# Kernel optimization log

Hardware: AMD Instinct MI355X
Metric: run time of the kernel (lower is better)

Reference implementation:

```python
import jax, jax.numpy as jnp
import numpy as np

N = 65536   # total nodes
E = 1048576 # total edges (avg degree 16)
B = 512     # graphs in batch
H = 4       # gat1 heads
C = 64      # per-head channels / GNN_HIDDEN


def segment_softmax(logits, seg, num_segments):
    # numerically stable softmax over segments (PyG softmax semantics, eps=1e-16)
    m = jax.ops.segment_max(logits, seg, num_segments=num_segments)
    m = jnp.where(jnp.isfinite(m), m, 0.0)
    e = jnp.exp(logits - m[seg])
    s = jax.ops.segment_sum(e, seg, num_segments=num_segments)
    return e / (s[seg] + 1e-16)


def gat_conv(x, edge_index, edge_attr, W, att_src, att_dst, We, att_edge, bias, heads, out_ch, concat):
    # PyG GATConv with edge_dim, add_self_loops=False
    n = x.shape[0]
    h = (x @ W).reshape(n, heads, out_ch)                 # (N,H,C)
    src, dst = edge_index[0], edge_index[1]
    a_s = jnp.sum(h * att_src, axis=-1)                   # (N,H)
    a_d = jnp.sum(h * att_dst, axis=-1)                   # (N,H)
    he = (edge_attr @ We).reshape(-1, heads, out_ch)      # (E,H,C)
    a_e = jnp.sum(he * att_edge, axis=-1)                 # (E,H)
    alpha = jax.nn.leaky_relu(a_s[src] + a_d[dst] + a_e, negative_slope=0.2)
    alpha = segment_softmax(alpha, dst, n)                # softmax over incoming edges per dst
    out = jax.ops.segment_sum(h[src] * alpha[..., None], dst, num_segments=n)  # (N,H,C)
    out = out.reshape(n, heads * out_ch) if concat else out.mean(axis=1)
    return out + bias


def setup_inputs() -> dict:
    key = jax.random.key(0)
    ks = jax.random.split(key, 24)
    s = 0.05
    d = {}
    d["global_feat"] = jax.random.normal(ks[0], (B, 512), jnp.float32)
    d["x"] = jax.random.normal(ks[1], (N, 13), jnp.float32)
    d["roi_feats"] = jax.random.normal(ks[2], (N, 256), jnp.float32)
    d["edge_index"] = jax.random.randint(ks[3], (2, E), 0, N)
    d["edge_attr"] = jax.random.normal(ks[4], (E, 5), jnp.float32)
    d["batch_vec"] = jnp.sort(jax.random.randint(ks[5], (N,), 0, B))
    # roi_proj / scene_proj
    d["roi_W"] = jax.random.normal(ks[6], (256, 64), jnp.float32) * s
    d["roi_b"] = jnp.zeros((64,), jnp.float32)
    d["scene_W"] = jax.random.normal(ks[7], (512, 128), jnp.float32) * s
    d["scene_b"] = jnp.zeros((128,), jnp.float32)
    d["g1_W"] = jax.random.normal(ks[8], (77, H * C), jnp.float32) * s
    d["g1_att_src"] = jax.random.normal(ks[9], (H, C), jnp.float32) * s
    d["g1_att_dst"] = jax.random.normal(ks[10], (H, C), jnp.float32) * s
    d["g1_We"] = jax.random.normal(ks[11], (5, H * C), jnp.float32) * s
    d["g1_att_edge"] = jax.random.normal(ks[12], (H, C), jnp.float32) * s
    d["g1_bias"] = jnp.zeros((H * C,), jnp.float32)
    # gat2: 256 -> 64, 1 head
    d["g2_W"] = jax.random.normal(ks[13], (H * C, C), jnp.float32) * s
    d["g2_att_src"] = jax.random.normal(ks[14], (1, C), jnp.float32) * s
    d["g2_att_dst"] = jax.random.normal(ks[15], (1, C), jnp.float32) * s
    d["g2_We"] = jax.random.normal(ks[16], (5, C), jnp.float32) * s
    d["g2_att_edge"] = jax.random.normal(ks[17], (1, C), jnp.float32) * s
    d["g2_bias"] = jnp.zeros((C,), jnp.float32)
    # attention pooling gate + classifier
    d["gate_W"] = jax.random.normal(ks[18], (C, 1), jnp.float32) * s
    d["gate_b"] = jnp.zeros((1,), jnp.float32)
    d["cls1_W"] = jax.random.normal(ks[19], (128 + C, 64), jnp.float32) * s
    d["cls1_b"] = jnp.zeros((64,), jnp.float32)
    d["cls2_W"] = jax.random.normal(ks[20], (64, 3), jnp.float32) * s
    d["cls2_b"] = jnp.zeros((3,), jnp.float32)
    return d


def reference(global_feat, x, roi_feats, edge_index, edge_attr, batch_vec,
              roi_W, roi_b, scene_W, scene_b,
              g1_W, g1_att_src, g1_att_dst, g1_We, g1_att_edge, g1_bias,
              g2_W, g2_att_src, g2_att_dst, g2_We, g2_att_edge, g2_bias,
              gate_W, gate_b, cls1_W, cls1_b, cls2_W, cls2_b):
    scene = global_feat @ scene_W + scene_b                       # (B,128)
    vis = jax.nn.relu(roi_feats @ roi_W + roi_b)                  # (N,64)
    h = jnp.concatenate([x, vis], axis=-1)                        # (N,77)
    h = jax.nn.relu(gat_conv(h, edge_index, edge_attr, g1_W, g1_att_src, g1_att_dst, g1_We, g1_att_edge, g1_bias, H, C, True))
    h = gat_conv(h, edge_index, edge_attr, g2_W, g2_att_src, g2_att_dst, g2_We, g2_att_edge, g2_bias, 1, C, False)  # (N,64)
    # GlobalAttention pooling
    gate = segment_softmax((h @ gate_W + gate_b)[:, 0], batch_vec, B)
    rel = jax.ops.segment_sum(gate[:, None] * h, batch_vec, num_segments=B)  # (B,64)
    comb = jnp.concatenate([scene, rel], axis=-1)                 # (B,192)
    hid = jax.nn.relu(comb @ cls1_W + cls1_b)                     # dropout off (eval)
    return hid @ cls2_W + cls2_b                                  # (B,3)
```

## Files before the change

kernel.cpp:

```cpp
#include <hip/hip_runtime.h>

#define N_NODES 65536
#define N_EDGES 1048576
#define NB      512

typedef unsigned short u16;
typedef unsigned int   u32;
typedef unsigned long long u64;

typedef __attribute__((ext_vector_type(8))) short bf16x8;
typedef __attribute__((ext_vector_type(4))) float f32x4;

__device__ __forceinline__ float bf2f(u16 u) { return __uint_as_float(((u32)u) << 16); }
__device__ __forceinline__ float lo16(u32 u) { return __uint_as_float(u << 16); }
__device__ __forceinline__ float hi16(u32 u) { return __uint_as_float(u & 0xffff0000u); }
__device__ __forceinline__ u16 f2bf(float f) {
    u32 u = __float_as_uint(f);
    u32 r = (u + 0x7fffu + ((u >> 16) & 1u)) >> 16;
    return (u16)r;
}
__device__ __forceinline__ u32 pk2(float a, float b) {
    return (u32)f2bf(a) | ((u32)f2bf(b) << 16);
}
__device__ __forceinline__ float wsum(float v) {
    for (int o = 32; o; o >>= 1) v += __shfl_xor(v, o, 64);
    return v;
}
__device__ __forceinline__ float wmax(float v) {
    for (int o = 32; o; o >>= 1) v = fmaxf(v, __shfl_xor(v, o, 64));
    return v;
}

__global__ void k_prep(const float* g1We, const float* g1ae, const float* g2We, const float* g2ae,
                       float* M1, float* M2) {
    int t = threadIdx.x;
    if (t < 20) {
        int j = t >> 2, h = t & 3;
        float s = 0.f;
        for (int c = 0; c < 64; c++) s += g1We[j * 256 + h * 64 + c] * g1ae[h * 64 + c];
        M1[t] = s;
    } else if (t < 25) {
        int j = t - 20;
        float s = 0.f;
        for (int c = 0; c < 64; c++) s += g2We[j * 64 + c] * g2ae[c];
        M2[j] = s;
    }
}

__global__ void k_wt1(const float* __restrict__ g1W, u16* __restrict__ Wt) {
    int c = blockIdx.x;
    int k = threadIdx.x;
    float v = 0.f;
    if (k < 77) {
        int ko = (k < 64) ? (13 + k) : (k - 64);
        v = g1W[(size_t)ko * 256 + c];
    }
    Wt[(size_t)c * 96 + k] = f2bf(v);
}

__global__ void k_wtv(const float* __restrict__ W, u16* __restrict__ Wt) {
    int c = blockIdx.x;
    int k = threadIdx.x;
    Wt[(size_t)c * 256 + k] = f2bf(W[(size_t)k * 64 + c]);
}

__global__ __launch_bounds__(256) void k_scene(const float* __restrict__ gf, const float* __restrict__ W,
                                               const float* __restrict__ bias, float* __restrict__ scene) {
    int idx = blockIdx.x * 256 + threadIdx.x;
    int b = idx >> 7, j = idx & 127;
    float acc = 0.f;
    for (int k = 0; k < 512; k++) acc += gf[b * 512 + k] * W[k * 128 + j];
    scene[idx] = acc + bias[j];
}

__global__ __launch_bounds__(256) void k_hist(const int* ei, int* cnt) {
    int e = blockIdx.x * 256 + threadIdx.x;
    atomicAdd(&cnt[ei[N_EDGES + e]], 1);
}

__global__ __launch_bounds__(256) void k_scan_blk(const int* __restrict__ cnt, int* __restrict__ pre,
                                                  int* __restrict__ bsum) {
    __shared__ int sd[256];
    int t = threadIdx.x, b = blockIdx.x;
    int base = b * 1024 + t * 4;
    int4 c = *(const int4*)(cnt + base);
    int s = c.x + c.y + c.z + c.w;
    sd[t] = s;
    __syncthreads();
    for (int off = 1; off < 256; off <<= 1) {
        int v = (t >= off) ? sd[t - off] : 0;
        __syncthreads();
        sd[t] += v;
        __syncthreads();
    }
    int excl = sd[t] - s;
    int4 p;
    p.x = excl;
    p.y = excl + c.x;
    p.z = excl + c.x + c.y;
    p.w = excl + c.x + c.y + c.z;
    *(int4*)(pre + base) = p;
    if (t == 255) bsum[b] = sd[255];
}

__global__ __launch_bounds__(64) void k_scan_top(int* bsum) {
    int t = threadIdx.x;
    int v = bsum[t];
    int inc = v;
    for (int off = 1; off < 64; off <<= 1) {
        int u = __shfl_up(inc, off, 64);
        if (t >= off) inc += u;
    }
    bsum[t] = inc - v;
}

__global__ __launch_bounds__(256) void k_scan_fix(const int* __restrict__ pre, const int* __restrict__ bsum,
                                                  int* __restrict__ row_ptr, int* __restrict__ coarse_cur) {
    int i = blockIdx.x * 256 + threadIdx.x;
    int v = pre[i] + bsum[i >> 10];
    row_ptr[i] = v;
    if ((i & 255) == 0) coarse_cur[i >> 8] = v;
    if (i == 0) row_ptr[N_NODES] = N_EDGES;
}

__global__ __launch_bounds__(256) void k_bucket(const int* __restrict__ ei, int* coarse_cur,
                                                u32* __restrict__ bpack, int* __restrict__ bsrc) {
    __shared__ u32 stageP[4096];
    __shared__ int stageS[4096];
    __shared__ int bcnt[256], bscan[256], boff[256], gbase[256];
    int t = threadIdx.x;
    int e0 = blockIdx.x * 4096;
    bcnt[t] = 0;
    __syncthreads();
    int dreg[16], sreg[16];
    for (int it = 0; it < 16; it++) {
        int e = e0 + it * 256 + t;
        int dd = ei[N_EDGES + e];
        dreg[it] = dd;
        sreg[it] = ei[e];
        atomicAdd(&bcnt[dd >> 8], 1);
    }
    __syncthreads();
    int v = bcnt[t];
    bscan[t] = v;
    __syncthreads();
    for (int off = 1; off < 256; off <<= 1) {
        int u = (t >= off) ? bscan[t - off] : 0;
        __syncthreads();
        bscan[t] += u;
        __syncthreads();
    }
    boff[t] = bscan[t] - v;
    gbase[t] = v ? atomicAdd(&coarse_cur[t], v) : 0;
    __syncthreads();
    for (int it = 0; it < 16; it++) {
        int e = e0 + it * 256 + t;
        int b = dreg[it] >> 8;
        int pos = atomicAdd(&boff[b], 1);
        stageP[pos] = ((u32)e << 12) | (u32)(dreg[it] & 255);
        stageS[pos] = sreg[it];
    }
    __syncthreads();
    for (int idx = t; idx < 4096; idx += 256) {
        int lo = 0, hi = 255;
        while (lo < hi) { int mid = (lo + hi) >> 1; if (bscan[mid] > idx) hi = mid; else lo = mid + 1; }
        int b = lo;
        int g = gbase[b] + (idx - (bscan[b] - bcnt[b]));
        bpack[g] = stageP[idx];
        bsrc[g] = stageS[idx];
    }
}

__global__ __launch_bounds__(256) void k_sortb(const u32* __restrict__ bpack, const int* __restrict__ bsrc,
                                               const int* __restrict__ row_ptr,
                                               int* __restrict__ eord, int* __restrict__ ssrc) {
    __shared__ int cur[256];
    int t = threadIdx.x, b = blockIdx.x;
    int nbase = b * 256;
    cur[t] = row_ptr[nbase + t];
    __syncthreads();
    int beg = row_ptr[nbase];
    int end = row_ptr[nbase + 256];
    for (int i = beg + t; i < end; i += 256) {
        u32 wd = bpack[i];
        int src = bsrc[i];
        int d8 = wd & 255;
        int pos = atomicAdd(&cur[d8], 1);
        eord[pos] = (int)(wd >> 12);
        ssrc[pos] = src;
    }
}

__global__ __launch_bounds__(256) void k_payload(const int* __restrict__ eord, const float* __restrict__ ea,
                                                 const float* __restrict__ M1, const float* __restrict__ M2,
                                                 float* __restrict__ a1es, float* __restrict__ a2es) {
    int pos = blockIdx.x * 256 + threadIdx.x;
    int e = eord[pos];
    float v[5];
    for (int j = 0; j < 5; j++) v[j] = ea[(size_t)e * 5 + j];
    float4 o;
    o.x = v[0]*M1[0]  + v[1]*M1[4]  + v[2]*M1[8]  + v[3]*M1[12] + v[4]*M1[16];
    o.y = v[0]*M1[1]  + v[1]*M1[5]  + v[2]*M1[9]  + v[3]*M1[13] + v[4]*M1[17];
    o.z = v[0]*M1[2]  + v[1]*M1[6]  + v[2]*M1[10] + v[3]*M1[14] + v[4]*M1[18];
    o.w = v[0]*M1[3]  + v[1]*M1[7]  + v[2]*M1[11] + v[3]*M1[15] + v[4]*M1[19];
    *(float4*)(a1es + (size_t)pos * 4) = o;
    a2es[pos] = v[0]*M2[0] + v[1]*M2[1] + v[2]*M2[2] + v[3]*M2[3] + v[4]*M2[4];
}

__global__ __launch_bounds__(256) void k_vis(const float* __restrict__ roi, const u16* __restrict__ Wt,
                                             const float* __restrict__ bias, u16* __restrict__ out) {
    __shared__ u16 At[64][264];
    int t = threadIdx.x;
    int w = t >> 6, l = t & 63, lo = l & 15, hi = l >> 4;
    int n0 = blockIdx.x * 64;
    int r = t >> 2, sub = t & 3;
    const float* rp = roi + (size_t)(n0 + r) * 256 + sub * 4;
    #pragma unroll
    for (int q = 0; q < 16; q++) {
        float4 v = *(const float4*)(rp + q * 16);
        uint2 p;
        p.x = pk2(v.x, v.y);
        p.y = pk2(v.z, v.w);
        *(uint2*)&At[r][q * 16 + sub * 4] = p;
    }
    float bb[4][4];
    #pragma unroll
    for (int cb = 0; cb < 4; cb++)
        #pragma unroll
        for (int rg = 0; rg < 4; rg++) bb[cb][rg] = bias[cb * 16 + hi * 4 + rg];
    __syncthreads();
    f32x4 acc[4];
    #pragma unroll
    for (int cb = 0; cb < 4; cb++) acc[cb] = (f32x4){0.f, 0.f, 0.f, 0.f};
    #pragma unroll
    for (int ks = 0; ks < 8; ks++) {
        bf16x8 af = *(const bf16x8*)(&At[w * 16 + lo][ks * 32 + hi * 8]);
        #pragma unroll
        for (int cb = 0; cb < 4; cb++) {
            bf16x8 wf = *(const bf16x8*)(Wt + (size_t)(cb * 16 + lo) * 256 + ks * 32 + hi * 8);
            acc[cb] = __builtin_amdgcn_mfma_f32_16x16x32_bf16(wf, af, acc[cb], 0, 0, 0);
        }
    }
    int nrow = n0 + w * 16 + lo;
    #pragma unroll
    for (int cb = 0; cb < 4; cb++) {
        uint2 p;
        p.x = pk2(fmaxf(acc[cb][0] + bb[cb][0], 0.f), fmaxf(acc[cb][1] + bb[cb][1], 0.f));
        p.y = pk2(fmaxf(acc[cb][2] + bb[cb][2], 0.f), fmaxf(acc[cb][3] + bb[cb][3], 0.f));
        *(uint2*)(out + (size_t)nrow * 64 + cb * 16 + hi * 4) = p;
    }
}

__global__ __launch_bounds__(256) void k_h1(const float* __restrict__ x, const u16* __restrict__ vis,
                                            const u16* __restrict__ Wt,
                                            const float* __restrict__ as_, const float* __restrict__ ad_,
                                            u16* __restrict__ h1, float* __restrict__ a1s,
                                            float* __restrict__ a1d) {
    __shared__ u16 At[64][104];
    int t = threadIdx.x;
    int w = t >> 6, l = t & 63, lo = l & 15, hi = l >> 4;
    int n0 = blockIdx.x * 64;
    int r = t >> 2, sub = t & 3;
    {
        const uint4* vp = (const uint4*)(vis + (size_t)(n0 + r) * 64 + sub * 16);
        uint4 v0 = vp[0], v1 = vp[1];
        *(uint4*)&At[r][sub * 16] = v0;
        *(uint4*)&At[r][sub * 16 + 8] = v1;
        if (sub == 0) {
            const float* xp = x + (size_t)(n0 + r) * 13;
            #pragma unroll
            for (int j = 0; j < 13; j++) At[r][64 + j] = f2bf(xp[j]);
        } else if (sub == 1) {
            #pragma unroll
            for (int j = 77; j < 96; j++) At[r][j] = 0;
        }
    }
    bf16x8 wf[4][3];
    float asv[4][4], adv[4][4];
    #pragma unroll
    for (int cb = 0; cb < 4; cb++) {
        #pragma unroll
        for (int ks = 0; ks < 3; ks++)
            wf[cb][ks] = *(const bf16x8*)(Wt + (size_t)(w * 64 + cb * 16 + lo) * 96 + ks * 32 + hi * 8);
        #pragma unroll
        for (int rg = 0; rg < 4; rg++) {
            asv[cb][rg] = as_[w * 64 + cb * 16 + hi * 4 + rg];
            adv[cb][rg] = ad_[w * 64 + cb * 16 + hi * 4 + rg];
        }
    }
    __syncthreads();
    #pragma unroll
    for (int nb = 0; nb < 4; nb++) {
        f32x4 acc[4];
        #pragma unroll
        for (int cb = 0; cb < 4; cb++) acc[cb] = (f32x4){0.f, 0.f, 0.f, 0.f};
        #pragma unroll
        for (int ks = 0; ks < 3; ks++) {
            bf16x8 af = *(const bf16x8*)(&At[nb * 16 + lo][ks * 32 + hi * 8]);
            #pragma unroll
            for (int cb = 0; cb < 4; cb++)
                acc[cb] = __builtin_amdgcn_mfma_f32_16x16x32_bf16(wf[cb][ks], af, acc[cb], 0, 0, 0);
        }
        int nrow = n0 + nb * 16 + lo;
        float ps = 0.f, pd = 0.f;
        #pragma unroll
        for (int cb = 0; cb < 4; cb++) {
            uint2 p;
            p.x = pk2(acc[cb][0], acc[cb][1]);
            p.y = pk2(acc[cb][2], acc[cb][3]);
            *(uint2*)(h1 + (size_t)nrow * 256 + w * 64 + cb * 16 + hi * 4) = p;
            ps += acc[cb][0] * asv[cb][0] + acc[cb][1] * asv[cb][1]
                + acc[cb][2] * asv[cb][2] + acc[cb][3] * asv[cb][3];
            pd += acc[cb][0] * adv[cb][0] + acc[cb][1] * adv[cb][1]
                + acc[cb][2] * adv[cb][2] + acc[cb][3] * adv[cb][3];
        }
        ps += __shfl_xor(ps, 16, 64); ps += __shfl_xor(ps, 32, 64);
        pd += __shfl_xor(pd, 16, 64); pd += __shfl_xor(pd, 32, 64);
        if (hi == 0) {
            a1s[nrow * 4 + w] = ps;
            a1d[nrow * 4 + w] = pd;
        }
    }
}

__global__ __launch_bounds__(256) void k_h2(const u16* __restrict__ A, const u16* __restrict__ Wt,
                                            const float* __restrict__ as_, const float* __restrict__ ad_,
                                            u16* __restrict__ out, float* __restrict__ a2s,
                                            float* __restrict__ a2d) {
    int t = threadIdx.x;
    int w = t >> 6, l = t & 63, lo = l & 15, hi = l >> 4;
    int nrow = blockIdx.x * 64 + w * 16 + lo;
    f32x4 acc[4];
    #pragma unroll
    for (int cb = 0; cb < 4; cb++) acc[cb] = (f32x4){0.f, 0.f, 0.f, 0.f};
    const u16* ap = A + (size_t)nrow * 256 + hi * 8;
    #pragma unroll
    for (int ks = 0; ks < 8; ks++) {
        bf16x8 af = *(const bf16x8*)(ap + ks * 32);
        #pragma unroll
        for (int cb = 0; cb < 4; cb++) {
            bf16x8 wf = *(const bf16x8*)(Wt + (size_t)(cb * 16 + lo) * 256 + ks * 32 + hi * 8);
            acc[cb] = __builtin_amdgcn_mfma_f32_16x16x32_bf16(wf, af, acc[cb], 0, 0, 0);
        }
    }
    float ps = 0.f, pd = 0.f;
    #pragma unroll
    for (int cb = 0; cb < 4; cb++) {
        uint2 p;
        p.x = pk2(acc[cb][0], acc[cb][1]);
        p.y = pk2(acc[cb][2], acc[cb][3]);
        *(uint2*)(out + (size_t)nrow * 64 + cb * 16 + hi * 4) = p;
        #pragma unroll
        for (int rg = 0; rg < 4; rg++) {
            float a = acc[cb][rg];
            ps += a * as_[cb * 16 + hi * 4 + rg];
            pd += a * ad_[cb * 16 + hi * 4 + rg];
        }
    }
    ps += __shfl_xor(ps, 16, 64); ps += __shfl_xor(ps, 32, 64);
    pd += __shfl_xor(pd, 16, 64); pd += __shfl_xor(pd, 32, 64);
    if (hi == 0) {
        a2s[nrow] = ps;
        a2d[nrow] = pd;
    }
}

__global__ __launch_bounds__(256) void k_sg1(const int* __restrict__ row_ptr, const int* __restrict__ ssrc,
                                             const float* __restrict__ a1s, const float* __restrict__ a1d,
                                             const float* __restrict__ a1es, const u16* __restrict__ h1,
                                             const float* __restrict__ bias, u16* __restrict__ out1) {
    __shared__ float wl[4][1024];
    int t = threadIdx.x;
    int wv = t >> 6, L = t & 63;
    int n = blockIdx.x * 4 + wv;
    int beg = row_ptr[n], deg = row_ptr[n + 1] - beg;
    int lim = (deg < 256) ? deg : 256;
    {
        int h = L >> 4, j = L & 15;
        float adn = a1d[n * 4 + h];
        float m = -3.0e38f, s = 0.f;
        for (int i = j; i < deg; i += 16) {
            int pos = beg + i;
            float l = a1s[ssrc[pos] * 4 + h] + adn + a1es[(size_t)pos * 4 + h];
            l = (l > 0.f) ? l : 0.2f * l;
            if (i < 256) wl[wv][i * 4 + h] = l;
            if (l > m) { s = s * __expf(m - l) + 1.f; m = l; }
            else       { s += __expf(l - m); }
        }
        for (int o = 1; o < 16; o <<= 1) {
            float mo = __shfl_xor(m, o, 64), so = __shfl_xor(s, o, 64);
            float M = fmaxf(m, mo);
            s = s * __expf(m - M) + so * __expf(mo - M);
            m = M;
        }
        float inv = 1.f / (s + 1e-16f);
        for (int i = j; i < lim; i += 16)
            wl[wv][i * 4 + h] = __expf(wl[wv][i * 4 + h] - m) * inv;
    }
    __syncthreads();
    int halfE = L >> 5;
    int L32 = L & 31;
    int hd = L32 >> 3;
    float acc[8];
    #pragma unroll
    for (int j = 0; j < 8; j++) acc[j] = 0.f;
    int last = beg + deg - 1;
    for (int i = 0; i < deg; i += 8) {
        int iA = i + halfE, iB = i + 2 + halfE, iC = i + 4 + halfE, iD = i + 6 + halfE;
        bool vA = iA < deg, vB = iB < deg, vC = iC < deg, vD = iD < deg;
        int cA = vA ? beg + iA : last, cB = vB ? beg + iB : last;
        int cC = vC ? beg + iC : last, cD = vD ? beg + iD : last;
        int sA = ssrc[cA], sB = ssrc[cB], sC = ssrc[cC], sD = ssrc[cD];
        float wA = vA ? wl[wv][iA * 4 + hd] : 0.f;
        float wB = vB ? wl[wv][iB * 4 + hd] : 0.f;
        float wC = vC ? wl[wv][iC * 4 + hd] : 0.f;
        float wD = vD ? wl[wv][iD * 4 + hd] : 0.f;
        uint4 uA = *((const uint4*)(h1 + (size_t)sA * 256) + L32);
        uint4 uB = *((const uint4*)(h1 + (size_t)sB * 256) + L32);
        uint4 uC = *((const uint4*)(h1 + (size_t)sC * 256) + L32);
        uint4 uD = *((const uint4*)(h1 + (size_t)sD * 256) + L32);
        acc[0] += wA * lo16(uA.x) + wB * lo16(uB.x) + wC * lo16(uC.x) + wD * lo16(uD.x);
        acc[1] += wA * hi16(uA.x) + wB * hi16(uB.x) + wC * hi16(uC.x) + wD * hi16(uD.x);
        acc[2] += wA * lo16(uA.y) + wB * lo16(uB.y) + wC * lo16(uC.y) + wD * lo16(uD.y);
        acc[3] += wA * hi16(uA.y) + wB * hi16(uB.y) + wC * hi16(uC.y) + wD * hi16(uD.y);
        acc[4] += wA * lo16(uA.z) + wB * lo16(uB.z) + wC * lo16(uC.z) + wD * lo16(uD.z);
        acc[5] += wA * hi16(uA.z) + wB * hi16(uB.z) + wC * hi16(uC.z) + wD * hi16(uD.z);
        acc[6] += wA * lo16(uA.w) + wB * lo16(uB.w) + wC * lo16(uC.w) + wD * lo16(uD.w);
        acc[7] += wA * hi16(uA.w) + wB * hi16(uB.w) + wC * hi16(uC.w) + wD * hi16(uD.w);
    }
    #pragma unroll
    for (int j = 0; j < 8; j++) acc[j] += __shfl_xor(acc[j], 32, 64);
    if (halfE == 0) {
        float4 b0 = *(const float4*)(bias + 8 * L32);
        float4 b1 = *(const float4*)(bias + 8 * L32 + 4);
        uint4 pk;
        pk.x = (u32)f2bf(fmaxf(acc[0] + b0.x, 0.f)) | ((u32)f2bf(fmaxf(acc[1] + b0.y, 0.f)) << 16);
        pk.y = (u32)f2bf(fmaxf(acc[2] + b0.z, 0.f)) | ((u32)f2bf(fmaxf(acc[3] + b0.w, 0.f)) << 16);
        pk.z = (u32)f2bf(fmaxf(acc[4] + b1.x, 0.f)) | ((u32)f2bf(fmaxf(acc[5] + b1.y, 0.f)) << 16);
        pk.w = (u32)f2bf(fmaxf(acc[6] + b1.z, 0.f)) | ((u32)f2bf(fmaxf(acc[7] + b1.w, 0.f)) << 16);
        *((uint4*)(out1 + (size_t)n * 256) + L32) = pk;
    }
}

__global__ __launch_bounds__(256) void k_sg2(const int* __restrict__ row_ptr, const int* __restrict__ ssrc,
                                             const float* __restrict__ a2s, const float* __restrict__ a2d,
                                             const float* __restrict__ a2es, const u16* __restrict__ h2b,
                                             const float* __restrict__ bias, float* __restrict__ hfin) {
    __shared__ float wl[4][256];
    int t = threadIdx.x;
    int wv = t >> 6, L = t & 63;
    int n = blockIdx.x * 4 + wv;
    int beg = row_ptr[n], deg = row_ptr[n + 1] - beg;
    int lim = (deg < 256) ? deg : 256;
    {
        float adn = a2d[n];
        float m = -3.0e38f, s = 0.f;
        for (int i = L; i < deg; i += 64) {
            int pos = beg + i;
            float l = a2s[ssrc[pos]] + adn + a2es[pos];
            l = (l > 0.f) ? l : 0.2f * l;
            if (i < 256) wl[wv][i] = l;
            if (l > m) { s = s * __expf(m - l) + 1.f; m = l; }
            else       { s += __expf(l - m); }
        }
        for (int o = 1; o < 64; o <<= 1) {
            float mo = __shfl_xor(m, o, 64), so = __shfl_xor(s, o, 64);
            float M = fmaxf(m, mo);
            s = s * __expf(m - M) + so * __expf(mo - M);
            m = M;
        }
        float inv = 1.f / (s + 1e-16f);
        for (int i = L; i < lim; i += 64)
            wl[wv][i] = __expf(wl[wv][i] - m) * inv;
    }
    __syncthreads();
    int halfE = L >> 5;
    int L32 = L & 31;
    float a0 = 0.f, a1v = 0.f;
    int last = beg + deg - 1;
    const u32* h2u = (const u32*)h2b;
    for (int i = 0; i < deg; i += 8) {
        int iA = i + halfE, iB = i + 2 + halfE, iC = i + 4 + halfE, iD = i + 6 + halfE;
        bool vA = iA < deg, vB = iB < deg, vC = iC < deg, vD = iD < deg;
        int cA = vA ? beg + iA : last, cB = vB ? beg + iB : last;
        int cC = vC ? beg + iC : last, cD = vD ? beg + iD : last;
        int sA = ssrc[cA], sB = ssrc[cB], sC = ssrc[cC], sD = ssrc[cD];
        float wA = vA ? wl[wv][iA] : 0.f;
        float wB = vB ? wl[wv][iB] : 0.f;
        float wC = vC ? wl[wv][iC] : 0.f;
        float wD = vD ? wl[wv][iD] : 0.f;
        u32 uA = h2u[(size_t)sA * 32 + L32];
        u32 uB = h2u[(size_t)sB * 32 + L32];
        u32 uC = h2u[(size_t)sC * 32 + L32];
        u32 uD = h2u[(size_t)sD * 32 + L32];
        a0  += wA * lo16(uA) + wB * lo16(uB) + wC * lo16(uC) + wD * lo16(uD);
        a1v += wA * hi16(uA) + wB * hi16(uB) + wC * hi16(uC) + wD * hi16(uD);
    }
    a0  += __shfl_xor(a0, 32, 64);
    a1v += __shfl_xor(a1v, 32, 64);
    if (halfE == 0) {
        float2 o;
        o.x = a0  + bias[2 * L32];
        o.y = a1v + bias[2 * L32 + 1];
        *(float2*)(hfin + (size_t)n * 64 + 2 * L32) = o;
    }
}

__global__ __launch_bounds__(64) void k_pool(const int* __restrict__ bvec, const float* __restrict__ hf,
                                             const float* gateW, const float* gateb,
                                             const float* __restrict__ scene,
                                             const float* c1W, const float* c1b,
                                             const float* c2W, const float* c2b,
                                             float* __restrict__ outp) {
    int b = blockIdx.x, lane = threadIdx.x;
    __shared__ float gwl[64], se[64], comb[192], hid[64];
    gwl[lane] = gateW[lane];
    __syncthreads();
    int s0, s1;
    { int lo = 0, hi = N_NODES; while (lo < hi) { int mid = (lo + hi) >> 1; if (bvec[mid] < b) lo = mid + 1; else hi = mid; } s0 = lo; }
    { int lo = 0, hi = N_NODES; while (lo < hi) { int mid = (lo + hi) >> 1; if (bvec[mid] < b + 1) lo = mid + 1; else hi = mid; } s1 = lo; }
    float gb = gateb[0];
    float m = -3.0e38f, ssum = 0.f, acc = 0.f;
    for (int cs = s0; cs < s1; cs += 64) {
        int cnt = min(64, s1 - cs);
        float l = -3.0e38f;
        if (lane < cnt) {
            int n = cs + lane;
            float d = 0.f;
            for (int i = 0; i < 64; i++) d += hf[(size_t)n * 64 + i] * gwl[i];
            l = d + gb;
        }
        float cm = wmax(l);
        float newm = fmaxf(m, cm);
        float rsc = __expf(m - newm);
        float e = (lane < cnt) ? __expf(l - newm) : 0.f;
        float es = wsum(e);
        ssum = ssum * rsc + es;
        se[lane] = e;
        __syncthreads();
        float a2 = 0.f;
        for (int i = 0; i < cnt; i++) a2 += se[i] * hf[(size_t)(cs + i) * 64 + lane];
        acc = acc * rsc + a2;
        __syncthreads();
        m = newm;
    }
    float rel = acc / (ssum + 1e-16f);
    comb[lane] = scene[b * 128 + lane];
    comb[64 + lane] = scene[b * 128 + 64 + lane];
    comb[128 + lane] = rel;
    __syncthreads();
    float hj = 0.f;
    for (int k = 0; k < 192; k++) hj += comb[k] * c1W[k * 64 + lane];
    hj += c1b[lane];
    hid[lane] = fmaxf(hj, 0.f);
    __syncthreads();
    if (lane < 3) {
        float o = 0.f;
        for (int k = 0; k < 64; k++) o += hid[k] * c2W[k * 3 + lane];
        o += c2b[lane];
        outp[b * 3 + lane] = o;
    }
}

extern "C" void kernel_launch(void* const* d_in, const int* in_sizes, int n_in,
                              void* d_out, int out_size, void* d_ws, size_t ws_size,
                              hipStream_t stream) {
    (void)in_sizes; (void)n_in; (void)out_size; (void)ws_size;
    const float* gf     = (const float*)d_in[0];
    const float* x      = (const float*)d_in[1];
    const float* roi    = (const float*)d_in[2];
    const int*   ei     = (const int*)d_in[3];
    const float* ea     = (const float*)d_in[4];
    const int*   bvec   = (const int*)d_in[5];
    const float* roiW   = (const float*)d_in[6];
    const float* roib   = (const float*)d_in[7];
    const float* sceneW = (const float*)d_in[8];
    const float* sceneb = (const float*)d_in[9];
    const float* g1W    = (const float*)d_in[10];
    const float* g1as   = (const float*)d_in[11];
    const float* g1ad   = (const float*)d_in[12];
    const float* g1We   = (const float*)d_in[13];
    const float* g1ae   = (const float*)d_in[14];
    const float* g1b    = (const float*)d_in[15];
    const float* g2W    = (const float*)d_in[16];
    const float* g2as   = (const float*)d_in[17];
    const float* g2ad   = (const float*)d_in[18];
    const float* g2We   = (const float*)d_in[19];
    const float* g2ae   = (const float*)d_in[20];
    const float* g2b    = (const float*)d_in[21];
    const float* gateW  = (const float*)d_in[22];
    const float* gateb  = (const float*)d_in[23];
    const float* c1W    = (const float*)d_in[24];
    const float* c1b    = (const float*)d_in[25];
    const float* c2W    = (const float*)d_in[26];
    const float* c2b    = (const float*)d_in[27];

    char* w = (char*)d_ws;
    size_t o = 0;
    auto nxt = [&](size_t bytes) -> char* {
        char* p = w + o;
        o += (bytes + 255) & ~(size_t)255;
        return p;
    };
    float* scene  = (float*)nxt((size_t)NB * 128 * 4);
    float* M1     = (float*)nxt(80);
    float* M2     = (float*)nxt(32);
    u16* g1Wt     = (u16*)nxt((size_t)256 * 96 * 2);
    u16* roiWt    = (u16*)nxt((size_t)64 * 256 * 2);
    u16* g2Wt     = (u16*)nxt((size_t)64 * 256 * 2);
    int* cnt      = (int*)nxt((size_t)N_NODES * 4);
    int* pre      = (int*)nxt((size_t)N_NODES * 4);
    int* bsum     = (int*)nxt(64 * 4);
    int* row_ptr  = (int*)nxt((size_t)(N_NODES + 1) * 4);
    int* coarse   = (int*)nxt(256 * 4);
    u32* bpack    = (u32*)nxt((size_t)N_EDGES * 4);
    int* bsrc     = (int*)nxt((size_t)N_EDGES * 4);
    int* eord     = (int*)nxt((size_t)N_EDGES * 4);
    int* ssrc     = (int*)nxt((size_t)N_EDGES * 4);
    float* a1es   = (float*)nxt((size_t)N_EDGES * 16);
    float* a2es   = (float*)nxt((size_t)N_EDGES * 4);
    u16* visb     = (u16*)nxt((size_t)N_NODES * 64 * 2);
    u16* h1       = (u16*)nxt((size_t)N_NODES * 256 * 2);
    u16* out1     = (u16*)nxt((size_t)N_NODES * 256 * 2);
    u16* h2b      = (u16*)nxt((size_t)N_NODES * 64 * 2);
    float* hfin   = (float*)nxt((size_t)N_NODES * 64 * 4);
    float* a1s    = (float*)nxt((size_t)N_NODES * 16);
    float* a1d    = (float*)nxt((size_t)N_NODES * 16);
    float* a2s    = (float*)nxt((size_t)N_NODES * 4);
    float* a2d    = (float*)nxt((size_t)N_NODES * 4);

    hipMemsetAsync(cnt, 0, (size_t)N_NODES * 4, stream);
    k_prep<<<1, 32, 0, stream>>>(g1We, g1ae, g2We, g2ae, M1, M2);
    k_wt1<<<256, 96, 0, stream>>>(g1W, g1Wt);
    k_wtv<<<64, 256, 0, stream>>>(roiW, roiWt);
    k_wtv<<<64, 256, 0, stream>>>(g2W, g2Wt);
    k_scene<<<(NB * 128) / 256, 256, 0, stream>>>(gf, sceneW, sceneb, scene);
    k_hist<<<N_EDGES / 256, 256, 0, stream>>>(ei, cnt);
    k_scan_blk<<<64, 256, 0, stream>>>(cnt, pre, bsum);
    k_scan_top<<<1, 64, 0, stream>>>(bsum);
    k_scan_fix<<<N_NODES / 256, 256, 0, stream>>>(pre, bsum, row_ptr, coarse);
    k_bucket<<<256, 256, 0, stream>>>(ei, coarse, bpack, bsrc);
    k_sortb<<<256, 256, 0, stream>>>(bpack, bsrc, row_ptr, eord, ssrc);
    k_payload<<<N_EDGES / 256, 256, 0, stream>>>(eord, ea, M1, M2, a1es, a2es);
    k_vis<<<N_NODES / 64, 256, 0, stream>>>(roi, roiWt, roib, visb);
    k_h1<<<N_NODES / 64, 256, 0, stream>>>(x, visb, g1Wt, g1as, g1ad, h1, a1s, a1d);
    k_sg1<<<N_NODES / 4, 256, 0, stream>>>(row_ptr, ssrc, a1s, a1d, a1es, h1, g1b, out1);
    k_h2<<<N_NODES / 64, 256, 0, stream>>>(out1, g2Wt, g2as, g2ad, h2b, a2s, a2d);
    k_sg2<<<N_NODES / 4, 256, 0, stream>>>(row_ptr, ssrc, a2s, a2d, a2es, h2b, g2b, hfin);
    k_pool<<<NB, 64, 0, stream>>>(bvec, hfin, gateW, gateb, scene, c1W, c1b, c2W, c2b, (float*)d_out);
}
```

Before: 527.4 us.

## Aggregate raw input features before GAT1 projection and fold attention vectors into weights

Reorders the first GAT layer so messages aggregate the 77-wide (padded to 128) input features per head, then applies the W projection after aggregation (k_go1). The attention source and destination scores come from precomputed W·att vectors (k_prepv/k_a1) rather than from the projected features. The per-edge gather shrinks from 512 bytes of h1 to 256 bytes of featb, but this adds a per-node intermediate G of 4×128 bf16 values and an extra GEMM kernel. It also rounds intermediates differently, since attention is computed from bf16-rounded weights.

```diff
diff --git a/kernel.cpp b/kernel.cpp
--- a/kernel.cpp
+++ b/kernel.cpp
@@ -55,7 +55,22 @@
         int ko = (k < 64) ? (13 + k) : (k - 64);
         v = g1W[(size_t)ko * 256 + c];
     }
-    Wt[(size_t)c * 96 + k] = f2bf(v);
+    Wt[(size_t)c * 128 + k] = f2bf(v);
+}
+
+__global__ void k_prepv(const u16* __restrict__ Wt, const float* __restrict__ as_,
+                        const float* __restrict__ ad_, float* __restrict__ v1s,
+                        float* __restrict__ v1d) {
+    int t = threadIdx.x;
+    int h = t >> 7, k = t & 127;
+    float s = 0.f, d = 0.f;
+    for (int cc = 0; cc < 64; cc++) {
+        float wv_ = bf2f(Wt[(size_t)(h * 64 + cc) * 128 + k]);
+        s += wv_ * as_[h * 64 + cc];
+        d += wv_ * ad_[h * 64 + cc];
+    }
+    v1s[t] = s;
+    v1d[t] = d;
 }
 
 __global__ void k_wtv(const float* __restrict__ W, u16* __restrict__ Wt) {
@@ -208,7 +223,8 @@
 }
 
 __global__ __launch_bounds__(256) void k_vis(const float* __restrict__ roi, const u16* __restrict__ Wt,
-                                             const float* __restrict__ bias, u16* __restrict__ out) {
+                                             const float* __restrict__ bias, const float* __restrict__ x,
+                                             u16* __restrict__ featb) {
     __shared__ u16 At[64][264];
     int t = threadIdx.x;
     int w = t >> 6, l = t & 63, lo = l & 15, hi = l >> 4;
@@ -223,6 +239,18 @@
         p.y = pk2(v.z, v.w);
         *(uint2*)&At[r][q * 16 + sub * 4] = p;
     }
+    {
+        u16* fb = featb + (size_t)(n0 + r) * 128;
+        if (sub == 0) {
+            const float* xp = x + (size_t)(n0 + r) * 13;
+            #pragma unroll
+            for (int j = 0; j < 13; j++) fb[64 + j] = f2bf(xp[j]);
+        } else {
+            int j0 = 77 + (sub - 1) * 17;
+            #pragma unroll
+            for (int j = 0; j < 17; j++) fb[j0 + j] = 0;
+        }
+    }
     float bb[4][4];
     #pragma unroll
     for (int cb = 0; cb < 4; cb++)
@@ -247,128 +275,55 @@
         uint2 p;
         p.x = pk2(fmaxf(acc[cb][0] + bb[cb][0], 0.f), fmaxf(acc[cb][1] + bb[cb][1], 0.f));
         p.y = pk2(fmaxf(acc[cb][2] + bb[cb][2], 0.f), fmaxf(acc[cb][3] + bb[cb][3], 0.f));
-        *(uint2*)(out + (size_t)nrow * 64 + cb * 16 + hi * 4) = p;
-    }
-}
-
-__global__ __launch_bounds__(256) void k_h1(const float* __restrict__ x, const u16* __restrict__ vis,
-                                            const u16* __restrict__ Wt,
-                                            const float* __restrict__ as_, const float* __restrict__ ad_,
-                                            u16* __restrict__ h1, float* __restrict__ a1s,
-                                            float* __restrict__ a1d) {
-    __shared__ u16 At[64][104];
-    int t = threadIdx.x;
-    int w = t >> 6, l = t & 63, lo = l & 15, hi = l >> 4;
-    int n0 = blockIdx.x * 64;
-    int r = t >> 2, sub = t & 3;
-    {
-        const uint4* vp = (const uint4*)(vis + (size_t)(n0 + r) * 64 + sub * 16);
-        uint4 v0 = vp[0], v1 = vp[1];
-        *(uint4*)&At[r][sub * 16] = v0;
-        *(uint4*)&At[r][sub * 16 + 8] = v1;
-        if (sub == 0) {
-            const float* xp = x + (size_t)(n0 + r) * 13;
-            #pragma unroll
-            for (int j = 0; j < 13; j++) At[r][64 + j] = f2bf(xp[j]);
-        } else if (sub == 1) {
-            #pragma unroll
-            for (int j = 77; j < 96; j++) At[r][j] = 0;
-        }
-    }
-    bf16x8 wf[4][3];
-    float asv[4][4], adv[4][4];
-    #pragma unroll
-    for (int cb = 0; cb < 4; cb++) {
-        #pragma unroll
-        for (int ks = 0; ks < 3; ks++)
-            wf[cb][ks] = *(const bf16x8*)(Wt + (size_t)(w * 64 + cb * 16 + lo) * 96 + ks * 32 + hi * 8);
-        #pragma unroll
-        for (int rg = 0; rg < 4; rg++) {
-            asv[cb][rg] = as_[w * 64 + cb * 16 + hi * 4 + rg];
-            adv[cb][rg] = ad_[w * 64 + cb * 16 + hi * 4 + rg];
-        }
-    }
-    __syncthreads();
-    #pragma unroll
-    for (int nb = 0; nb < 4; nb++) {
-        f32x4 acc[4];
-        #pragma unroll
-        for (int cb = 0; cb < 4; cb++) acc[cb] = (f32x4){0.f, 0.f, 0.f, 0.f};
-        #pragma unroll
-        for (int ks = 0; ks < 3; ks++) {
-            bf16x8 af = *(const bf16x8*)(&At[nb * 16 + lo][ks * 32 + hi * 8]);
-            #pragma unroll
-            for (int cb = 0; cb < 4; cb++)
-                acc[cb] = __builtin_amdgcn_mfma_f32_16x16x32_bf16(wf[cb][ks], af, acc[cb], 0, 0, 0);
-        }
-        int nrow = n0 + nb * 16 + lo;
-        float ps = 0.f, pd = 0.f;
-        #pragma unroll
-        for (int cb = 0; cb < 4; cb++) {
-            uint2 p;
-            p.x = pk2(acc[cb][0], acc[cb][1]);
-            p.y = pk2(acc[cb][2], acc[cb][3]);
-            *(uint2*)(h1 + (size_t)nrow * 256 + w * 64 + cb * 16 + hi * 4) = p;
-            ps += acc[cb][0] * asv[cb][0] + acc[cb][1] * asv[cb][1]
-                + acc[cb][2] * asv[cb][2] + acc[cb][3] * asv[cb][3];
-            pd += acc[cb][0] * adv[cb][0] + acc[cb][1] * adv[cb][1]
-                + acc[cb][2] * adv[cb][2] + acc[cb][3] * adv[cb][3];
-        }
-        ps += __shfl_xor(ps, 16, 64); ps += __shfl_xor(ps, 32, 64);
-        pd += __shfl_xor(pd, 16, 64); pd += __shfl_xor(pd, 32, 64);
-        if (hi == 0) {
-            a1s[nrow * 4 + w] = ps;
-            a1d[nrow * 4 + w] = pd;
-        }
-    }
-}
-
-__global__ __launch_bounds__(256) void k_h2(const u16* __restrict__ A, const u16* __restrict__ Wt,
-                                            const float* __restrict__ as_, const float* __restrict__ ad_,
-                                            u16* __restrict__ out, float* __restrict__ a2s,
-                                            float* __restrict__ a2d) {
-    int t = threadIdx.x;
-    int w = t >> 6, l = t & 63, lo = l & 15, hi = l >> 4;
-    int nrow = blockIdx.x * 64 + w * 16 + lo;
-    f32x4 acc[4];
-    #pragma unroll
-    for (int cb = 0; cb < 4; cb++) acc[cb] = (f32x4){0.f, 0.f, 0.f, 0.f};
-    const u16* ap = A + (size_t)nrow * 256 + hi * 8;
-    #pragma unroll
-    for (int ks = 0; ks < 8; ks++) {
-        bf16x8 af = *(const bf16x8*)(ap + ks * 32);
-        #pragma unroll
-        for (int cb = 0; cb < 4; cb++) {
-            bf16x8 wf = *(const bf16x8*)(Wt + (size_t)(cb * 16 + lo) * 256 + ks * 32 + hi * 8);
-            acc[cb] = __builtin_amdgcn_mfma_f32_16x16x32_bf16(wf, af, acc[cb], 0, 0, 0);
-        }
-    }
-    float ps = 0.f, pd = 0.f;
-    #pragma unroll
-    for (int cb = 0; cb < 4; cb++) {
-        uint2 p;
-        p.x = pk2(acc[cb][0], acc[cb][1]);
-        p.y = pk2(acc[cb][2], acc[cb][3]);
-        *(uint2*)(out + (size_t)nrow * 64 + cb * 16 + hi * 4) = p;
-        #pragma unroll
-        for (int rg = 0; rg < 4; rg++) {
-            float a = acc[cb][rg];
-            ps += a * as_[cb * 16 + hi * 4 + rg];
-            pd += a * ad_[cb * 16 + hi * 4 + rg];
-        }
-    }
-    ps += __shfl_xor(ps, 16, 64); ps += __shfl_xor(ps, 32, 64);
-    pd += __shfl_xor(pd, 16, 64); pd += __shfl_xor(pd, 32, 64);
-    if (hi == 0) {
-        a2s[nrow] = ps;
-        a2d[nrow] = pd;
-    }
-}
-
-__global__ __launch_bounds__(256) void k_sg1(const int* __restrict__ row_ptr, const int* __restrict__ ssrc,
-                                             const float* __restrict__ a1s, const float* __restrict__ a1d,
-                                             const float* __restrict__ a1es, const u16* __restrict__ h1,
-                                             const float* __restrict__ bias, u16* __restrict__ out1) {
+        *(uint2*)(featb + (size_t)nrow * 128 + cb * 16 + hi * 4) = p;
+    }
+}
+
+__global__ __launch_bounds__(256) void k_a1(const u16* __restrict__ featb, const float* __restrict__ v1s,
+                                            const float* __restrict__ v1d,
+                                            float* __restrict__ a1s, float* __restrict__ a1d) {
+    __shared__ float vs[512], vd[512];
+    int t = threadIdx.x;
+    for (int idx = t; idx < 512; idx += 256) { vs[idx] = v1s[idx]; vd[idx] = v1d[idx]; }
+    __syncthreads();
+    int n = blockIdx.x * 32 + (t >> 3), l8 = t & 7;
+    const uint4* fp = (const uint4*)(featb + (size_t)n * 128 + l8 * 16);
+    uint4 u0 = fp[0], u1 = fp[1];
+    float f[16];
+    f[0]=lo16(u0.x); f[1]=hi16(u0.x); f[2]=lo16(u0.y); f[3]=hi16(u0.y);
+    f[4]=lo16(u0.z); f[5]=hi16(u0.z); f[6]=lo16(u0.w); f[7]=hi16(u0.w);
+    f[8]=lo16(u1.x); f[9]=hi16(u1.x); f[10]=lo16(u1.y); f[11]=hi16(u1.y);
+    f[12]=lo16(u1.z); f[13]=hi16(u1.z); f[14]=lo16(u1.w); f[15]=hi16(u1.w);
+    float as4[4], ad4[4];
+    #pragma unroll
+    for (int h = 0; h < 4; h++) {
+        float s = 0.f, d = 0.f;
+        #pragma unroll
+        for (int q = 0; q < 4; q++) {
+            float4 v4 = *(const float4*)&vs[h * 128 + l8 * 16 + q * 4];
+            float4 w4 = *(const float4*)&vd[h * 128 + l8 * 16 + q * 4];
+            s += f[q*4+0]*v4.x + f[q*4+1]*v4.y + f[q*4+2]*v4.z + f[q*4+3]*v4.w;
+            d += f[q*4+0]*w4.x + f[q*4+1]*w4.y + f[q*4+2]*w4.z + f[q*4+3]*w4.w;
+        }
+        as4[h] = s; ad4[h] = d;
+    }
+    #pragma unroll
+    for (int h = 0; h < 4; h++) {
+        for (int o = 1; o < 8; o <<= 1) {
+            as4[h] += __shfl_xor(as4[h], o, 64);
+            ad4[h] += __shfl_xor(ad4[h], o, 64);
+        }
+    }
+    if (l8 == 0) {
+        *(float4*)(a1s + (size_t)n * 4) = make_float4(as4[0], as4[1], as4[2], as4[3]);
+        *(float4*)(a1d + (size_t)n * 4) = make_float4(ad4[0], ad4[1], ad4[2], ad4[3]);
+    }
+}
+
+__global__ __launch_bounds__(256) void k_sg1g(const int* __restrict__ row_ptr, const int* __restrict__ ssrc,
+                                              const float* __restrict__ a1s, const float* __restrict__ a1d,
+                                              const float* __restrict__ a1es, const u16* __restrict__ featb,
+                                              u16* __restrict__ G) {
     __shared__ float wl[4][1024];
     int t = threadIdx.x;
     int wv = t >> 6, L = t & 63;
@@ -398,47 +353,130 @@
             wl[wv][i * 4 + h] = __expf(wl[wv][i * 4 + h] - m) * inv;
     }
     __syncthreads();
-    int halfE = L >> 5;
-    int L32 = L & 31;
-    int hd = L32 >> 3;
-    float acc[8];
-    #pragma unroll
-    for (int j = 0; j < 8; j++) acc[j] = 0.f;
-    int last = beg + deg - 1;
-    for (int i = 0; i < deg; i += 8) {
-        int iA = i + halfE, iB = i + 2 + halfE, iC = i + 4 + halfE, iD = i + 6 + halfE;
-        bool vA = iA < deg, vB = iB < deg, vC = iC < deg, vD = iD < deg;
-        int cA = vA ? beg + iA : last, cB = vB ? beg + iB : last;
-        int cC = vC ? beg + iC : last, cD = vD ? beg + iD : last;
-        int sA = ssrc[cA], sB = ssrc[cB], sC = ssrc[cC], sD = ssrc[cD];
-        float wA = vA ? wl[wv][iA * 4 + hd] : 0.f;
-        float wB = vB ? wl[wv][iB * 4 + hd] : 0.f;
-        float wC = vC ? wl[wv][iC * 4 + hd] : 0.f;
-        float wD = vD ? wl[wv][iD * 4 + hd] : 0.f;
-        uint4 uA = *((const uint4*)(h1 + (size_t)sA * 256) + L32);
-        uint4 uB = *((const uint4*)(h1 + (size_t)sB * 256) + L32);
-        uint4 uC = *((const uint4*)(h1 + (size_t)sC * 256) + L32);
-        uint4 uD = *((const uint4*)(h1 + (size_t)sD * 256) + L32);
-        acc[0] += wA * lo16(uA.x) + wB * lo16(uB.x) + wC * lo16(uC.x) + wD * lo16(uD.x);
-        acc[1] += wA * hi16(uA.x) + wB * hi16(uB.x) + wC * hi16(uC.x) + wD * hi16(uD.x);
-        acc[2] += wA * lo16(uA.y) + wB * lo16(uB.y) + wC * lo16(uC.y) + wD * lo16(uD.y);
-        acc[3] += wA * hi16(uA.y) + wB * hi16(uB.y) + wC * hi16(uC.y) + wD * hi16(uD.y);
-        acc[4] += wA * lo16(uA.z) + wB * lo16(uB.z) + wC * lo16(uC.z) + wD * lo16(uD.z);
-        acc[5] += wA * hi16(uA.z) + wB * hi16(uB.z) + wC * hi16(uC.z) + wD * hi16(uD.z);
-        acc[6] += wA * lo16(uA.w) + wB * lo16(uB.w) + wC * lo16(uC.w) + wD * lo16(uD.w);
-        acc[7] += wA * hi16(uA.w) + wB * hi16(uB.w) + wC * hi16(uC.w) + wD * hi16(uD.w);
-    }
-    #pragma unroll
-    for (int j = 0; j < 8; j++) acc[j] += __shfl_xor(acc[j], 32, 64);
-    if (halfE == 0) {
-        float4 b0 = *(const float4*)(bias + 8 * L32);
-        float4 b1 = *(const float4*)(bias + 8 * L32 + 4);
-        uint4 pk;
-        pk.x = (u32)f2bf(fmaxf(acc[0] + b0.x, 0.f)) | ((u32)f2bf(fmaxf(acc[1] + b0.y, 0.f)) << 16);
-        pk.y = (u32)f2bf(fmaxf(acc[2] + b0.z, 0.f)) | ((u32)f2bf(fmaxf(acc[3] + b0.w, 0.f)) << 16);
-        pk.z = (u32)f2bf(fmaxf(acc[4] + b1.x, 0.f)) | ((u32)f2bf(fmaxf(acc[5] + b1.y, 0.f)) << 16);
-        pk.w = (u32)f2bf(fmaxf(acc[6] + b1.z, 0.f)) | ((u32)f2bf(fmaxf(acc[7] + b1.w, 0.f)) << 16);
-        *((uint4*)(out1 + (size_t)n * 256) + L32) = pk;
+    int es = L >> 4;
+    int cg = L & 15;
+    float acc[4][8];
+    #pragma unroll
+    for (int h = 0; h < 4; h++)
+        #pragma unroll
+        for (int j2 = 0; j2 < 8; j2++) acc[h][j2] = 0.f;
+    for (int i = 0; i < deg; i += 4) {
+        int ii = i + es;
+        bool v = ii < deg;
+        int pos = v ? beg + ii : beg;
+        int s = ssrc[pos];
+        float4 al = v ? *(const float4*)&wl[wv][ii * 4] : make_float4(0.f, 0.f, 0.f, 0.f);
+        uint4 u = *((const uint4*)(featb + (size_t)s * 128) + cg);
+        float f0 = lo16(u.x), f1 = hi16(u.x), f2 = lo16(u.y), f3 = hi16(u.y);
+        float f4 = lo16(u.z), f5 = hi16(u.z), f6 = lo16(u.w), f7 = hi16(u.w);
+        #pragma unroll
+        for (int h = 0; h < 4; h++) {
+            float a = (&al.x)[h];
+            acc[h][0] += a * f0; acc[h][1] += a * f1;
+            acc[h][2] += a * f2; acc[h][3] += a * f3;
+            acc[h][4] += a * f4; acc[h][5] += a * f5;
+            acc[h][6] += a * f6; acc[h][7] += a * f7;
+        }
+    }
+    #pragma unroll
+    for (int h = 0; h < 4; h++)
+        #pragma unroll
+        for (int j2 = 0; j2 < 8; j2++) {
+            acc[h][j2] += __shfl_xor(acc[h][j2], 16, 64);
+            acc[h][j2] += __shfl_xor(acc[h][j2], 32, 64);
+        }
+    if (es == 0) {
+        #pragma unroll
+        for (int h = 0; h < 4; h++) {
+            uint4 p;
+            p.x = pk2(acc[h][0], acc[h][1]);
+            p.y = pk2(acc[h][2], acc[h][3]);
+            p.z = pk2(acc[h][4], acc[h][5]);
+            p.w = pk2(acc[h][6], acc[h][7]);
+            *((uint4*)(G + ((size_t)n * 4 + h) * 128) + cg) = p;
+        }
+    }
+}
+
+__global__ __launch_bounds__(256) void k_go1(const u16* __restrict__ G, const u16* __restrict__ Wt,
+                                             const float* __restrict__ bias, u16* __restrict__ out1) {
+    int t = threadIdx.x;
+    int w = t >> 6, l = t & 63, lo = l & 15, hi = l >> 4;
+    int n0 = blockIdx.x * 64;
+    bf16x8 wf[4][4];
+    float bb[4][4];
+    #pragma unroll
+    for (int cb = 0; cb < 4; cb++) {
+        #pragma unroll
+        for (int ks = 0; ks < 4; ks++)
+            wf[cb][ks] = *(const bf16x8*)(Wt + (size_t)(w * 64 + cb * 16 + lo) * 128 + ks * 32 + hi * 8);
+        #pragma unroll
+        for (int rg = 0; rg < 4; rg++)
+            bb[cb][rg] = bias[w * 64 + cb * 16 + hi * 4 + rg];
+    }
+    #pragma unroll
+    for (int nb = 0; nb < 4; nb++) {
+        f32x4 acc[4];
+        #pragma unroll
+        for (int cb = 0; cb < 4; cb++) acc[cb] = (f32x4){0.f, 0.f, 0.f, 0.f};
+        int nrow = n0 + nb * 16 + lo;
+        const u16* gp = G + ((size_t)nrow * 4 + w) * 128 + hi * 8;
+        #pragma unroll
+        for (int ks = 0; ks < 4; ks++) {
+            bf16x8 af = *(const bf16x8*)(gp + ks * 32);
+            #pragma unroll
+            for (int cb = 0; cb < 4; cb++)
+                acc[cb] = __builtin_amdgcn_mfma_f32_16x16x32_bf16(wf[cb][ks], af, acc[cb], 0, 0, 0);
+        }
+        #pragma unroll
+        for (int cb = 0; cb < 4; cb++) {
+            uint2 p;
+            p.x = pk2(fmaxf(acc[cb][0] + bb[cb][0], 0.f), fmaxf(acc[cb][1] + bb[cb][1], 0.f));
+            p.y = pk2(fmaxf(acc[cb][2] + bb[cb][2], 0.f), fmaxf(acc[cb][3] + bb[cb][3], 0.f));
+            *(uint2*)(out1 + (size_t)nrow * 256 + w * 64 + cb * 16 + hi * 4) = p;
+        }
+    }
+}
+
+__global__ __launch_bounds__(256) void k_h2(const u16* __restrict__ A, const u16* __restrict__ Wt,
+                                            const float* __restrict__ as_, const float* __restrict__ ad_,
+                                            u16* __restrict__ out, float* __restrict__ a2s,
+                                            float* __restrict__ a2d) {
+    int t = threadIdx.x;
+    int w = t >> 6, l = t & 63, lo = l & 15, hi = l >> 4;
+    int nrow = blockIdx.x * 64 + w * 16 + lo;
+    f32x4 acc[4];
+    #pragma unroll
+    for (int cb = 0; cb < 4; cb++) acc[cb] = (f32x4){0.f, 0.f, 0.f, 0.f};
+    const u16* ap = A + (size_t)nrow * 256 + hi * 8;
+    #pragma unroll
+    for (int ks = 0; ks < 8; ks++) {
+        bf16x8 af = *(const bf16x8*)(ap + ks * 32);
+        #pragma unroll
+        for (int cb = 0; cb < 4; cb++) {
+            bf16x8 wf = *(const bf16x8*)(Wt + (size_t)(cb * 16 + lo) * 256 + ks * 32 + hi * 8);
+            acc[cb] = __builtin_amdgcn_mfma_f32_16x16x32_bf16(wf, af, acc[cb], 0, 0, 0);
+        }
+    }
+    float ps = 0.f, pd = 0.f;
+    #pragma unroll
+    for (int cb = 0; cb < 4; cb++) {
+        uint2 p;
+        p.x = pk2(acc[cb][0], acc[cb][1]);
+        p.y = pk2(acc[cb][2], acc[cb][3]);
+        *(uint2*)(out + (size_t)nrow * 64 + cb * 16 + hi * 4) = p;
+        #pragma unroll
+        for (int rg = 0; rg < 4; rg++) {
+            float a = acc[cb][rg];
+            ps += a * as_[cb * 16 + hi * 4 + rg];
+            pd += a * ad_[cb * 16 + hi * 4 + rg];
+        }
+    }
+    ps += __shfl_xor(ps, 16, 64); ps += __shfl_xor(ps, 32, 64);
+    pd += __shfl_xor(pd, 16, 64); pd += __shfl_xor(pd, 32, 64);
+    if (hi == 0) {
+        a2s[nrow] = ps;
+        a2d[nrow] = pd;
     }
 }
 
@@ -605,9 +643,11 @@
     float* scene  = (float*)nxt((size_t)NB * 128 * 4);
     float* M1     = (float*)nxt(80);
     float* M2     = (float*)nxt(32);
-    u16* g1Wt     = (u16*)nxt((size_t)256 * 96 * 2);
+    u16* g1Wt     = (u16*)nxt((size_t)256 * 128 * 2);
     u16* roiWt    = (u16*)nxt((size_t)64 * 256 * 2);
     u16* g2Wt     = (u16*)nxt((size_t)64 * 256 * 2);
+    float* v1s    = (float*)nxt(512 * 4);
+    float* v1d    = (float*)nxt(512 * 4);
     int* cnt      = (int*)nxt((size_t)N_NODES * 4);
     int* pre      = (int*)nxt((size_t)N_NODES * 4);
     int* bsum     = (int*)nxt(64 * 4);
@@ -619,8 +659,8 @@
     int* ssrc     = (int*)nxt((size_t)N_EDGES * 4);
     float* a1es   = (float*)nxt((size_t)N_EDGES * 16);
     float* a2es   = (float*)nxt((size_t)N_EDGES * 4);
-    u16* visb     = (u16*)nxt((size_t)N_NODES * 64 * 2);
-    u16* h1       = (u16*)nxt((size_t)N_NODES * 256 * 2);
+    u16* featb    = (u16*)nxt((size_t)N_NODES * 128 * 2);
+    u16* G        = (u16*)nxt((size_t)N_NODES * 4 * 128 * 2);
     u16* out1     = (u16*)nxt((size_t)N_NODES * 256 * 2);
     u16* h2b      = (u16*)nxt((size_t)N_NODES * 64 * 2);
     float* hfin   = (float*)nxt((size_t)N_NODES * 64 * 4);
@@ -631,7 +671,8 @@
 
     hipMemsetAsync(cnt, 0, (size_t)N_NODES * 4, stream);
     k_prep<<<1, 32, 0, stream>>>(g1We, g1ae, g2We, g2ae, M1, M2);
-    k_wt1<<<256, 96, 0, stream>>>(g1W, g1Wt);
+    k_wt1<<<256, 128, 0, stream>>>(g1W, g1Wt);
+    k_prepv<<<1, 512, 0, stream>>>(g1Wt, g1as, g1ad, v1s, v1d);
     k_wtv<<<64, 256, 0, stream>>>(roiW, roiWt);
     k_wtv<<<64, 256, 0, stream>>>(g2W, g2Wt);
     k_scene<<<(NB * 128) / 256, 256, 0, stream>>>(gf, sceneW, sceneb, scene);
@@ -642,9 +683,10 @@
     k_bucket<<<256, 256, 0, stream>>>(ei, coarse, bpack, bsrc);
     k_sortb<<<256, 256, 0, stream>>>(bpack, bsrc, row_ptr, eord, ssrc);
     k_payload<<<N_EDGES / 256, 256, 0, stream>>>(eord, ea, M1, M2, a1es, a2es);
-    k_vis<<<N_NODES / 64, 256, 0, stream>>>(roi, roiWt, roib, visb);
-    k_h1<<<N_NODES / 64, 256, 0, stream>>>(x, visb, g1Wt, g1as, g1ad, h1, a1s, a1d);
-    k_sg1<<<N_NODES / 4, 256, 0, stream>>>(row_ptr, ssrc, a1s, a1d, a1es, h1, g1b, out1);
+    k_vis<<<N_NODES / 64, 256, 0, stream>>>(roi, roiWt, roib, x, featb);
+    k_a1<<<N_NODES / 32, 256, 0, stream>>>(featb, v1s, v1d, a1s, a1d);
+    k_sg1g<<<N_NODES / 4, 256, 0, stream>>>(row_ptr, ssrc, a1s, a1d, a1es, featb, G);
+    k_go1<<<N_NODES / 64, 256, 0, stream>>>(G, g1Wt, g1b, out1);
     k_h2<<<N_NODES / 64, 256, 0, stream>>>(out1, g2Wt, g2as, g2ad, h2b, a2s, a2d);
     k_sg2<<<N_NODES / 4, 256, 0, stream>>>(row_ptr, ssrc, a2s, a2d, a2es, h2b, g2b, hfin);
     k_pool<<<NB, 64, 0, stream>>>(bvec, hfin, gateW, gateb, scene, c1W, c1b, c2W, c2b, (float*)d_out);
```

New measurement: 550.9 us. +4.5%, slower.
